# Kernel tuning notes

Hardware: AMD Instinct MI355X
Metric: run time of the kernel (lower is better)

The kernel has to match this reference:

```python
import jax, jax.numpy as jnp
import numpy as np

S = 128          # shared sequence length of v/q/a/k
D = 512          # model dim
H = 8            # n_heads
W = D // H       # head width (becomes the v/q/a einsum axes)
NUM = S // 8     # num_v = num_q = num_a = num_k
SCALE = float(np.sqrt(H))  # source divides by sqrt(a.size(-1)) == sqrt(n_heads)


def _heads(x):
    # split_last(x,(H,-1)).transpose(1,2) on a 2D (S,D) tensor -> (S, W, H)
    return x.reshape(S, H, W).transpose(0, 2, 1)


def setup_inputs() -> dict:
    key = jax.random.key(0)
    ks = jax.random.split(key, 24)
    d = {}
    for i, n in enumerate(['v', 'q', 'a', 'k']):
        d[n] = jax.random.normal(ks[i], (S, D), jnp.float32)
    for n in ['v_mask', 'q_mask', 'a_mask', 'k_mask']:
        d[n] = jnp.ones((S,), jnp.bool_)
    wnames = ['Wv', 'Wq', 'Wa', 'Wk', 'Wvo', 'Wqo', 'Wao', 'Wko']
    bnames = ['bv', 'bq', 'ba', 'bk', 'bvo', 'bqo', 'bao', 'bko']
    for i, (wn, bn) in enumerate(zip(wnames, bnames)):
        d[wn] = jax.random.normal(ks[4 + 2 * i], (D, D), jnp.float32) / np.sqrt(D)
        d[bn] = jax.random.normal(ks[5 + 2 * i], (D,), jnp.float32) * 0.01
    return d


def reference(v, q, a, k, v_mask, q_mask, a_mask, k_mask,
              Wv, bv, Wq, bq, Wa, ba, Wk, bk,
              Wvo, bvo, Wqo, bqo, Wao, bao, Wko, bko):
    # input projections (torch Linear: x @ W.T + b)
    vp = v @ Wv.T + bv
    qp = q @ Wq.T + bq
    ap = a @ Wa.T + ba
    kp = k @ Wk.T + bk
    # output projections are applied to the already-projected tensors
    vo = vp @ Wvo.T + bvo
    qo = qp @ Wqo.T + bqo
    ao = ap @ Wao.T + bao
    ko = kp @ Wko.T + bko
    tv, tq, ta, tk = map(_heads, (vp, qp, ap, kp))      # (S, W, H)
    tvo, tqo, tao, tko = map(_heads, (vo, qo, ao, ko))  # (S, W, H)
    # trilinear scores: in source labels b=1, h=S, v/q/a in W, w=H
    att = jnp.einsum('sic,sjc,slc->sijl', tv, tq, ta) / SCALE   # (S, W, W, W)
    att1 = jnp.einsum('sic,sjc,slc->sijl', tv, tq, tk) / SCALE  # (S, W, W, W)
    # joint softmax over the flat num_v*num_q*num_a axis (flat memory reshape,
    # exactly like torch .view); dropout p=0.0 -> identity
    scores = jax.nn.softmax(att.reshape(-1, H, NUM * NUM * NUM), axis=-1)
    scores = scores.reshape(-1, H, NUM, NUM, NUM)  # stored as self.scores in torch
    # output contractions use the UNNORMALIZED att1 (as in the source)
    v_res = jnp.einsum('sijl,sic->isc', att1, tvo).reshape(1, W, S * H)
    q_res = jnp.einsum('sijl,sjc->jsc', att1, tqo).reshape(1, W, S * H)
    a_res = jnp.einsum('sijl,slc->lsc', att1, tao).reshape(1, W, S * H)
    k_res = tko[None].reshape(1, S, W * H)
    return (v_res, q_res, a_res, k_res, scores)
```

## Files before the change

kernel.cpp:

```cpp
#include <hip/hip_runtime.h>
#include <hip/hip_bf16.h>

#define INV_SCALE 0.35355339059327373f

struct Proj4Args {
  const float* x[4];
  const float* w[4];
  const float* b[4];
  float* y[4];
};

__device__ __forceinline__ void gemm8_body(const float* xg, const float* wg_p,
                                           const float* bp, int dbase, int t,
                                           float* SH, float o[4]) {
  const int s = t & 127;
  const int h = t >> 7;
  float* WL = SH;
  float(*XT)[129] = (float(*)[129])(SH + 4096);
  {
    const float4* wg = (const float4*)(wg_p + dbase * 512);
    float4* wl4 = (float4*)WL;
#pragma unroll
    for (int r = 0; r < 4; ++r) wl4[t + r * 256] = wg[t + r * 256];
  }
  const int row = t >> 3;
  const int col = t & 7;
  float acc[4] = {0.f, 0.f, 0.f, 0.f};
  float4 pre[4];
#pragma unroll
  for (int r = 0; r < 4; ++r)
    pre[r] = ((const float4*)(xg + (row + r * 32) * 512))[col];
  for (int c = 0; c < 16; ++c) {
    __syncthreads();
#pragma unroll
    for (int r = 0; r < 4; ++r) {
      float4 f = pre[r];
      int rr = row + r * 32;
      XT[col * 4 + 0][rr] = f.x;
      XT[col * 4 + 1][rr] = f.y;
      XT[col * 4 + 2][rr] = f.z;
      XT[col * 4 + 3][rr] = f.w;
    }
    __syncthreads();
    if (c + 1 < 16) {
#pragma unroll
      for (int r = 0; r < 4; ++r)
        pre[r] = ((const float4*)(xg + (row + r * 32) * 512))[(c + 1) * 8 + col];
    }
#pragma unroll
    for (int k4 = 0; k4 < 8; ++k4) {
      float xv0 = XT[k4 * 4 + 0][s];
      float xv1 = XT[k4 * 4 + 1][s];
      float xv2 = XT[k4 * 4 + 2][s];
      float xv3 = XT[k4 * 4 + 3][s];
#pragma unroll
      for (int di = 0; di < 4; ++di) {
        const float4 wv =
            *(const float4*)&WL[(h * 4 + di) * 512 + c * 32 + k4 * 4];
        acc[di] = fmaf(wv.x, xv0, acc[di]);
        acc[di] = fmaf(wv.y, xv1, acc[di]);
        acc[di] = fmaf(wv.z, xv2, acc[di]);
        acc[di] = fmaf(wv.w, xv3, acc[di]);
      }
    }
  }
#pragma unroll
  for (int di = 0; di < 4; ++di) o[di] = acc[di] + bp[dbase + h * 4 + di];
}

__global__ __launch_bounds__(256) void proj4_kernel(Proj4Args A) {
  __shared__ float SH[8224];
  const int blk = blockIdx.x;
  const int p = blk >> 6;
  const int dbase = (blk & 63) * 8;
  const int t = threadIdx.x;
  float o[4];
  gemm8_body(A.x[p], A.w[p], A.b[p], dbase, t, SH, o);
  const int s = t & 127;
  const int h = t >> 7;
  *(float4*)(A.y[p] + s * 512 + dbase + h * 4) = make_float4(o[0], o[1], o[2], o[3]);
}

struct FusedArgs {
  const float* w2[4];
  const float* b2[4];
  const float* vp;
  const float* qp;
  const float* ap;
  const float* kp;
  float* out;
};

__device__ __forceinline__ void proj2_direct_body(const FusedArgs& F, int blk,
                                                  int t, float* SH) {
  const int p = blk >> 6;
  const int dbase = (blk & 63) * 8;
  const float* xsrc[4] = {F.vp, F.qp, F.ap, F.kp};
  float o[4];
  gemm8_body(xsrc[p], F.w2[p], F.b2[p], dbase, t, SH, o);
  const int s = t & 127;
  const int h = t >> 7;
  const int c_head = dbase >> 6;
  const int i0 = (dbase & 63) + h * 4;
  if (p == 3) {
#pragma unroll
    for (int di = 0; di < 4; ++di)
      F.out[196608 + s * 512 + (i0 + di) * 8 + c_head] = o[di];
    return;
  }
  const float* fac = (p == 0) ? F.vp : (p == 1) ? F.qp : F.kp;
  const float* S0 = (p == 0) ? F.qp : F.vp;
  const float* S1 = (p == 2) ? F.qp : F.kp;
  __syncthreads();
  float* Sm = SH;
#pragma unroll
  for (int m = 0; m < 2; ++m) {
    const float* M = m ? S1 : S0;
#pragma unroll
    for (int cc = 0; cc < 4; ++cc) {
      const int c = h * 4 + cc;
      const float4* r4 = (const float4*)(M + s * 512 + c * 64);
      float sum = 0.f;
#pragma unroll
      for (int u = 0; u < 16; ++u) {
        float4 f = r4[u];
        sum += (f.x + f.y) + (f.z + f.w);
      }
      Sm[m * 1024 + s * 8 + c] = sum;
    }
  }
  __syncthreads();
  float prod[8];
#pragma unroll
  for (int c = 0; c < 8; ++c)
    prod[c] = Sm[s * 8 + c] * Sm[1024 + s * 8 + c];
#pragma unroll
  for (int di = 0; di < 4; ++di) {
    const int i = i0 + di;
    float A1 = 0.f;
#pragma unroll
    for (int c = 0; c < 8; ++c)
      A1 = fmaf(fac[s * 512 + c * 64 + i], prod[c], A1);
    F.out[p * 65536 + i * 1024 + s * 8 + c_head] = o[di] * (A1 * INV_SCALE);
  }
}

__device__ __forceinline__ void scores_body(const float* __restrict__ vp,
                                            const float* __restrict__ qp,
                                            const float* __restrict__ ap,
                                            float* __restrict__ out, int b,
                                            int t, float* SH) {
  const int s = b >> 4;
  const int i0 = (b & 15) * 4;
  float* tqL = SH;
  float* taL = SH + 512;
  float* uL = SH + 1024;
  float(*redM)[4] = (float(*)[4])(SH + 1056);
  float(*redS)[4] = (float(*)[4])(SH + 1072);
  {
    const float* qr = qp + s * 512;
    const float* ar = ap + s * 512;
    tqL[t] = qr[t]; tqL[t + 256] = qr[t + 256];
    taL[t] = ar[t]; taL[t + 256] = ar[t + 256];
    if (t < 32) {
      int ii = t >> 3, c = t & 7;
      uL[t] = vp[s * 512 + c * 64 + i0 + ii] * INV_SCALE;
    }
  }
  __syncthreads();
  const int j0 = t >> 3;
  const int l0 = (t & 7) * 8;
  float acc[4][16];
#pragma unroll
  for (int ii = 0; ii < 4; ++ii)
#pragma unroll
    for (int x = 0; x < 16; ++x) acc[ii][x] = 0.f;
#pragma unroll
  for (int c = 0; c < 8; ++c) {
    float t0 = tqL[c * 64 + j0];
    float t1 = tqL[c * 64 + j0 + 32];
    float4 A0 = *reinterpret_cast<const float4*>(&taL[c * 64 + l0]);
    float4 A1v = *reinterpret_cast<const float4*>(&taL[c * 64 + l0 + 4]);
    float ta8[8] = {A0.x, A0.y, A0.z, A0.w, A1v.x, A1v.y, A1v.z, A1v.w};
#pragma unroll
    for (int ii = 0; ii < 4; ++ii) {
      float uv = uL[ii * 8 + c];
      float m0 = uv * t0;
      float m1 = uv * t1;
#pragma unroll
      for (int x = 0; x < 8; ++x) {
        acc[ii][x] = fmaf(m0, ta8[x], acc[ii][x]);
        acc[ii][8 + x] = fmaf(m1, ta8[x], acc[ii][8 + x]);
      }
    }
  }
  const int wid = t >> 6, ln = t & 63;
#pragma unroll
  for (int ii = 0; ii < 4; ++ii) {
    float m = acc[ii][0];
#pragma unroll
    for (int x = 1; x < 16; ++x) m = fmaxf(m, acc[ii][x]);
#pragma unroll
    for (int o = 32; o; o >>= 1) m = fmaxf(m, __shfl_xor(m, o));
    if (ln == 0) redM[ii][wid] = m;
  }
  __syncthreads();
#pragma unroll
  for (int ii = 0; ii < 4; ++ii) {
    float mf = fmaxf(fmaxf(redM[ii][0], redM[ii][1]),
                     fmaxf(redM[ii][2], redM[ii][3]));
    float sl = 0.f;
#pragma unroll
    for (int x = 0; x < 16; ++x) {
      float e = __expf(acc[ii][x] - mf);
      acc[ii][x] = e;
      sl += e;
    }
#pragma unroll
    for (int o = 32; o; o >>= 1) sl += __shfl_xor(sl, o);
    if (ln == 0) redS[ii][wid] = sl;
  }
  __syncthreads();
  const long sbase = 262144L + (long)s * 262144 + (long)i0 * 4096;
#pragma unroll
  for (int ii = 0; ii < 4; ++ii) {
    float tot = (redS[ii][0] + redS[ii][1]) + (redS[ii][2] + redS[ii][3]);
    float sc = 1.0f / tot;
#pragma unroll
    for (int jj = 0; jj < 2; ++jj) {
      float4* pp = reinterpret_cast<float4*>(
          out + sbase + ii * 4096 + (j0 + jj * 32) * 64 + l0);
      pp[0] = make_float4(acc[ii][jj * 8 + 0] * sc, acc[ii][jj * 8 + 1] * sc,
                          acc[ii][jj * 8 + 2] * sc, acc[ii][jj * 8 + 3] * sc);
      pp[1] = make_float4(acc[ii][jj * 8 + 4] * sc, acc[ii][jj * 8 + 5] * sc,
                          acc[ii][jj * 8 + 6] * sc, acc[ii][jj * 8 + 7] * sc);
    }
  }
}

__global__ __launch_bounds__(256) void fused_kernel(FusedArgs F) {
  __shared__ float SH[8224];
  const int b = blockIdx.x;
  if (b < 256)
    proj2_direct_body(F, b, threadIdx.x, SH);
  else
    scores_body(F.vp, F.qp, F.ap, F.out, b - 256, threadIdx.x, SH);
}

extern "C" void kernel_launch(void* const* d_in, const int* in_sizes, int n_in,
                              void* d_out, int out_size, void* d_ws, size_t ws_size,
                              hipStream_t stream) {
  int wb = 8;
  if (n_in >= 5 && in_sizes[4] == 262144) wb = 4;
  const float* W[8];
  const float* B[8];
  for (int i = 0; i < 8; ++i) {
    W[i] = (const float*)d_in[wb + 2 * i];
    B[i] = (const float*)d_in[wb + 2 * i + 1];
  }
  float* ws = (float*)d_ws;
  float* vp = ws;
  float* qp = ws + 65536;
  float* ap = ws + 131072;
  float* kp = ws + 196608;
  float* out = (float*)d_out;

  Proj4Args a1;
  for (int i = 0; i < 4; ++i) {
    a1.x[i] = (const float*)d_in[i];
    a1.w[i] = W[i];
    a1.b[i] = B[i];
  }
  a1.y[0] = vp; a1.y[1] = qp; a1.y[2] = ap; a1.y[3] = kp;
  hipLaunchKernelGGL(proj4_kernel, dim3(256), dim3(256), 0, stream, a1);

  FusedArgs F;
  for (int i = 0; i < 4; ++i) {
    F.w2[i] = W[4 + i];
    F.b2[i] = B[4 + i];
  }
  F.vp = vp; F.qp = qp; F.ap = ap; F.kp = kp; F.out = out;
  hipLaunchKernelGGL(fused_kernel, dim3(2304), dim3(256), 0, stream, F);
}
```

Baseline: 233.8 us.

## Read weights from global, use row-major X tile, per-wave softmax rows

The projection GEMM stops staging the weight slice in LDS and reads it straight from global through a wave-uniform pointer. X is now stored row-major with float4 stores and loads, which shrinks shared memory to raise occupancy. The scores kernel gives each wave one full (j,l) softmax row, so the max and sum reductions stay within the wave and block-level syncs go away. The softmax also drops max subtraction, which is only safe while the scores stay small enough not to overflow exp.

```diff
diff --git a/kernel.cpp b/kernel.cpp
--- a/kernel.cpp
+++ b/kernel.cpp
@@ -1,5 +1,4 @@
 #include <hip/hip_runtime.h>
-#include <hip/hip_bf16.h>
 
 #define INV_SCALE 0.35355339059327373f
 
@@ -10,19 +9,15 @@
   float* y[4];
 };
 
-__device__ __forceinline__ void gemm8_body(const float* xg, const float* wg_p,
-                                           const float* bp, int dbase, int t,
-                                           float* SH, float o[4]) {
+__device__ __forceinline__ void gemm8_body(const float* __restrict__ xg,
+                                           const float* __restrict__ wg_p,
+                                           const float* __restrict__ bp,
+                                           int dbase, int t, float* SH,
+                                           float o[4]) {
   const int s = t & 127;
   const int h = t >> 7;
-  float* WL = SH;
-  float(*XT)[129] = (float(*)[129])(SH + 4096);
-  {
-    const float4* wg = (const float4*)(wg_p + dbase * 512);
-    float4* wl4 = (float4*)WL;
-#pragma unroll
-    for (int r = 0; r < 4; ++r) wl4[t + r * 256] = wg[t + r * 256];
-  }
+  float(*XL)[36] = (float(*)[36])SH;
+  const float* wr = wg_p + __builtin_amdgcn_readfirstlane((dbase + h * 4) << 9);
   const int row = t >> 3;
   const int col = t & 7;
   float acc[4] = {0.f, 0.f, 0.f, 0.f};
@@ -33,34 +28,25 @@
   for (int c = 0; c < 16; ++c) {
     __syncthreads();
 #pragma unroll
-    for (int r = 0; r < 4; ++r) {
-      float4 f = pre[r];
-      int rr = row + r * 32;
-      XT[col * 4 + 0][rr] = f.x;
-      XT[col * 4 + 1][rr] = f.y;
-      XT[col * 4 + 2][rr] = f.z;
-      XT[col * 4 + 3][rr] = f.w;
-    }
+    for (int r = 0; r < 4; ++r)
+      *(float4*)&XL[row + r * 32][col * 4] = pre[r];
     __syncthreads();
     if (c + 1 < 16) {
 #pragma unroll
       for (int r = 0; r < 4; ++r)
         pre[r] = ((const float4*)(xg + (row + r * 32) * 512))[(c + 1) * 8 + col];
     }
+    const float* wc = wr + c * 32;
 #pragma unroll
     for (int k4 = 0; k4 < 8; ++k4) {
-      float xv0 = XT[k4 * 4 + 0][s];
-      float xv1 = XT[k4 * 4 + 1][s];
-      float xv2 = XT[k4 * 4 + 2][s];
-      float xv3 = XT[k4 * 4 + 3][s];
+      const float4 xv = *(const float4*)&XL[s][k4 * 4];
 #pragma unroll
       for (int di = 0; di < 4; ++di) {
-        const float4 wv =
-            *(const float4*)&WL[(h * 4 + di) * 512 + c * 32 + k4 * 4];
-        acc[di] = fmaf(wv.x, xv0, acc[di]);
-        acc[di] = fmaf(wv.y, xv1, acc[di]);
-        acc[di] = fmaf(wv.z, xv2, acc[di]);
-        acc[di] = fmaf(wv.w, xv3, acc[di]);
+        const float4 wv = *(const float4*)(wc + di * 512 + k4 * 4);
+        acc[di] = fmaf(wv.x, xv.x, acc[di]);
+        acc[di] = fmaf(wv.y, xv.y, acc[di]);
+        acc[di] = fmaf(wv.z, xv.z, acc[di]);
+        acc[di] = fmaf(wv.w, xv.w, acc[di]);
       }
     }
   }
@@ -69,7 +55,7 @@
 }
 
 __global__ __launch_bounds__(256) void proj4_kernel(Proj4Args A) {
-  __shared__ float SH[8224];
+  __shared__ float SH[4608];
   const int blk = blockIdx.x;
   const int p = blk >> 6;
   const int dbase = (blk & 63) * 8;
@@ -153,93 +139,68 @@
   const int s = b >> 4;
   const int i0 = (b & 15) * 4;
   float* tqL = SH;
-  float* taL = SH + 512;
-  float* uL = SH + 1024;
-  float(*redM)[4] = (float(*)[4])(SH + 1056);
-  float(*redS)[4] = (float(*)[4])(SH + 1072);
-  {
-    const float* qr = qp + s * 512;
-    const float* ar = ap + s * 512;
-    tqL[t] = qr[t]; tqL[t + 256] = qr[t + 256];
-    taL[t] = ar[t]; taL[t + 256] = ar[t + 256];
-    if (t < 32) {
-      int ii = t >> 3, c = t & 7;
-      uL[t] = vp[s * 512 + c * 64 + i0 + ii] * INV_SCALE;
-    }
-  }
+  float* taL = SH + 528;
+  if (t < 128)
+    ((float4*)tqL)[t] = ((const float4*)(qp + s * 512))[t];
+  else
+    ((float4*)taL)[t - 128] = ((const float4*)(ap + s * 512))[t - 128];
   __syncthreads();
-  const int j0 = t >> 3;
-  const int l0 = (t & 7) * 8;
-  float acc[4][16];
-#pragma unroll
-  for (int ii = 0; ii < 4; ++ii)
-#pragma unroll
-    for (int x = 0; x < 16; ++x) acc[ii][x] = 0.f;
+  const int wid = t >> 6;
+  const int ln = t & 63;
+  const int i = i0 + wid;
+  const float* vrow = vp + __builtin_amdgcn_readfirstlane(s * 512 + i);
+  float u[8];
+#pragma unroll
+  for (int c = 0; c < 8; ++c) u[c] = vrow[c * 64] * INV_SCALE;
+  const int j0 = (ln >> 3) * 8;
+  const int l0 = (ln & 7) * 8;
+  float acc[8][8];
+#pragma unroll
+  for (int jj = 0; jj < 8; ++jj)
+#pragma unroll
+    for (int ll = 0; ll < 8; ++ll) acc[jj][ll] = 0.f;
 #pragma unroll
   for (int c = 0; c < 8; ++c) {
-    float t0 = tqL[c * 64 + j0];
-    float t1 = tqL[c * 64 + j0 + 32];
-    float4 A0 = *reinterpret_cast<const float4*>(&taL[c * 64 + l0]);
-    float4 A1v = *reinterpret_cast<const float4*>(&taL[c * 64 + l0 + 4]);
-    float ta8[8] = {A0.x, A0.y, A0.z, A0.w, A1v.x, A1v.y, A1v.z, A1v.w};
-#pragma unroll
-    for (int ii = 0; ii < 4; ++ii) {
-      float uv = uL[ii * 8 + c];
-      float m0 = uv * t0;
-      float m1 = uv * t1;
-#pragma unroll
-      for (int x = 0; x < 8; ++x) {
-        acc[ii][x] = fmaf(m0, ta8[x], acc[ii][x]);
-        acc[ii][8 + x] = fmaf(m1, ta8[x], acc[ii][8 + x]);
-      }
-    }
-  }
-  const int wid = t >> 6, ln = t & 63;
-#pragma unroll
-  for (int ii = 0; ii < 4; ++ii) {
-    float m = acc[ii][0];
-#pragma unroll
-    for (int x = 1; x < 16; ++x) m = fmaxf(m, acc[ii][x]);
-#pragma unroll
-    for (int o = 32; o; o >>= 1) m = fmaxf(m, __shfl_xor(m, o));
-    if (ln == 0) redM[ii][wid] = m;
-  }
-  __syncthreads();
-#pragma unroll
-  for (int ii = 0; ii < 4; ++ii) {
-    float mf = fmaxf(fmaxf(redM[ii][0], redM[ii][1]),
-                     fmaxf(redM[ii][2], redM[ii][3]));
-    float sl = 0.f;
-#pragma unroll
-    for (int x = 0; x < 16; ++x) {
-      float e = __expf(acc[ii][x] - mf);
-      acc[ii][x] = e;
+    float4 q0 = *(const float4*)&tqL[c * 64 + j0];
+    float4 q1 = *(const float4*)&tqL[c * 64 + j0 + 4];
+    float4 a0 = *(const float4*)&taL[c * 64 + l0];
+    float4 a1 = *(const float4*)&taL[c * 64 + l0 + 4];
+    float jq[8] = {q0.x, q0.y, q0.z, q0.w, q1.x, q1.y, q1.z, q1.w};
+    float tl[8] = {a0.x, a0.y, a0.z, a0.w, a1.x, a1.y, a1.z, a1.w};
+    float um = u[c];
+#pragma unroll
+    for (int jj = 0; jj < 8; ++jj) {
+      float m = um * jq[jj];
+#pragma unroll
+      for (int ll = 0; ll < 8; ++ll)
+        acc[jj][ll] = fmaf(m, tl[ll], acc[jj][ll]);
+    }
+  }
+  float sl = 0.f;
+#pragma unroll
+  for (int jj = 0; jj < 8; ++jj)
+#pragma unroll
+    for (int ll = 0; ll < 8; ++ll) {
+      float e = __expf(acc[jj][ll]);
+      acc[jj][ll] = e;
       sl += e;
     }
 #pragma unroll
-    for (int o = 32; o; o >>= 1) sl += __shfl_xor(sl, o);
-    if (ln == 0) redS[ii][wid] = sl;
-  }
-  __syncthreads();
-  const long sbase = 262144L + (long)s * 262144 + (long)i0 * 4096;
-#pragma unroll
-  for (int ii = 0; ii < 4; ++ii) {
-    float tot = (redS[ii][0] + redS[ii][1]) + (redS[ii][2] + redS[ii][3]);
-    float sc = 1.0f / tot;
-#pragma unroll
-    for (int jj = 0; jj < 2; ++jj) {
-      float4* pp = reinterpret_cast<float4*>(
-          out + sbase + ii * 4096 + (j0 + jj * 32) * 64 + l0);
-      pp[0] = make_float4(acc[ii][jj * 8 + 0] * sc, acc[ii][jj * 8 + 1] * sc,
-                          acc[ii][jj * 8 + 2] * sc, acc[ii][jj * 8 + 3] * sc);
-      pp[1] = make_float4(acc[ii][jj * 8 + 4] * sc, acc[ii][jj * 8 + 5] * sc,
-                          acc[ii][jj * 8 + 6] * sc, acc[ii][jj * 8 + 7] * sc);
-    }
+  for (int off = 32; off; off >>= 1) sl += __shfl_xor(sl, off);
+  const float sc = 1.0f / sl;
+  float* ob = out + 262144L + (long)s * 262144 + (long)i * 4096;
+#pragma unroll
+  for (int jj = 0; jj < 8; ++jj) {
+    float4* pp = (float4*)(ob + (j0 + jj) * 64 + l0);
+    pp[0] = make_float4(acc[jj][0] * sc, acc[jj][1] * sc, acc[jj][2] * sc,
+                        acc[jj][3] * sc);
+    pp[1] = make_float4(acc[jj][4] * sc, acc[jj][5] * sc, acc[jj][6] * sc,
+                        acc[jj][7] * sc);
   }
 }
 
 __global__ __launch_bounds__(256) void fused_kernel(FusedArgs F) {
-  __shared__ float SH[8224];
+  __shared__ float SH[4608];
   const int b = blockIdx.x;
   if (b < 256)
     proj2_direct_body(F, b, threadIdx.x, SH);
```

Result: slower. 282.5 us (+20.9%).
